# Kernel optimization log

Measured on AMD Instinct MI355X. Metric: run time of the kernel, lower is better.

## Reference

```python
import jax, jax.numpy as jnp
import numpy as np


def get_grid_index(init_grid_size, map_size):
    # nearest-neighbor 'interpolation' of flat indices, matching F.interpolate(mode='nearest')
    H_init, W_init = init_grid_size
    H, W = map_size
    # torch nearest: src index = floor(dst * scale), scale = src/dst
    rows = jnp.floor(jnp.arange(H_init) * (H / H_init)).astype(jnp.int32)
    cols = jnp.floor(jnp.arange(W_init) * (W / W_init)).astype(jnp.int32)
    idx = rows[:, None] * W + cols[None, :]
    return idx.reshape(-1)  # [N_init]


def _map2token(feature_map, idx_token, N, H_init, W_init):
    B, C, H, W = feature_map.shape
    N_init = H_init * W_init
    idx_hw = get_grid_index((H_init, W_init), (H, W))  # [N_init]
    # gather per-grid feature values: fm_flat[b, idx_hw] -> [B, N_init, C]
    fm = feature_map.transpose(0, 2, 3, 1).reshape(B, H * W, C)
    src = fm[:, idx_hw, :]  # [B, N_init, C]
    # scatter-add into tokens with counts
    def scatter_b(src_b, idx_b):
        num = jnp.zeros((N, C), src_b.dtype).at[idx_b].add(src_b)
        cnt = jnp.zeros((N,), src_b.dtype).at[idx_b].add(1.0)
        return num / (cnt + 1e-6)[:, None]
    return jax.vmap(scatter_b)(src, idx_token)  # [B, N, C]


def _token2map(x, idx_token, H, W, H_init, W_init):
    B, N, C = x.shape
    N_init = H_init * W_init
    idx_hw = get_grid_index((H_init, W_init), (H, W))  # [N_init]
    # each initial grid point contributes token x[b, idx_token[b,i]] to map cell idx_hw[i]
    def scatter_b(x_b, idx_tok_b):
        src = x_b[idx_tok_b]  # [N_init, C]
        num = jnp.zeros((H * W, C), x_b.dtype).at[idx_hw].add(src)
        cnt = jnp.zeros((H * W,), x_b.dtype).at[idx_hw].add(1.0)
        return num / (cnt + 1e-6)[:, None]
    out = jax.vmap(scatter_b)(x, idx_token)  # [B, H*W, C]
    return out.reshape(B, H, W, C).transpose(0, 3, 1, 2)


def setup_inputs() -> dict:
    key = jax.random.key(0)
    k1, k2, k3 = jax.random.split(key, 3)
    B, C, H, W = 8, 256, 56, 56
    N = 784
    H_init = W_init = 56
    N_init = H_init * W_init
    feature_map = jax.random.normal(k1, (B, C, H, W), dtype=jnp.float32)
    x = jax.random.normal(k2, (B, N, C), dtype=jnp.float32)
    idx_token = jax.random.randint(k3, (B, N_init), 0, N)
    return {"feature_map": feature_map, "x": x, "idx_token": idx_token,
            "token_num": N, "map_H": H, "map_W": W, "init_H": H_init, "init_W": W_init}


def reference(feature_map, x, idx_token, token_num, map_H, map_W, init_H, init_W):
    tokens = _map2token(feature_map, idx_token, token_num, init_H, init_W)
    fmap = _token2map(x, idx_token, map_H, map_W, init_H, init_W)
    return tokens, fmap
```

## Files before the change

kernel.cpp:

```cpp
#include <hip/hip_runtime.h>

#define BATCH 8
#define CCH   256
#define HWSZ  3136
#define NTOK  784
#define NINIT 3136
#define MAXM  40

#define FMT_OFF   0
#define CNT_OFF   25690112
#define SLOT_OFF  (25690112 + 25600)

#define CSR_BLOCKS 8
#define TR_BLOCKS  (BATCH * 49)
#define FM_BLOCKS  (BATCH * 49)
#define D1_BLOCKS  (CSR_BLOCKS + TR_BLOCKS + FM_BLOCKS)

__global__ __launch_bounds__(256) void d1_kernel(
    const float* __restrict__ fm,
    const float* __restrict__ x,
    const int*   __restrict__ idx,
    float*       __restrict__ fmap,
    float*       __restrict__ fmT,
    int*         __restrict__ cnt,
    int*         __restrict__ slot)
{
    __shared__ __align__(16) float tile[64][65];
    __shared__ int ns[64];

    const int bid = blockIdx.x;
    const int tid = threadIdx.x;

    if (bid < CSR_BLOCKS) {
        int* cnt_s = (int*)tile;
        int* cur_s = ((int*)tile) + NTOK;
        const int b = bid;
        for (int n = tid; n < NTOK; n += 256) { cnt_s[n] = 0; cur_s[n] = 0; }
        __syncthreads();
        const int* ib = idx + b * NINIT;
        for (int i = tid; i < NINIT; i += 256) atomicAdd(&cnt_s[ib[i]], 1);
        __syncthreads();
        for (int n = tid; n < NTOK; n += 256) cnt[b * NTOK + n] = cnt_s[n];
        for (int i = tid; i < NINIT; i += 256) {
            const int n = ib[i];
            const int p = atomicAdd(&cur_s[n], 1);
            if (p < MAXM) slot[(b * NTOK + n) * MAXM + p] = i;
        }
    } else if (bid < CSR_BLOCKS + TR_BLOCKS) {
        int t = bid - CSR_BLOCKS;
        const int b  = t & 7;
        const int it = t >> 3;
        const int i0 = it * 64;
        const int q  = tid & 15;
        const int r0 = tid >> 4;

        for (int ct = 0; ct < 4; ++ct) {
            const int c0 = ct * 64;
            #pragma unroll
            for (int p = 0; p < 4; ++p) {
                const int r = r0 + p * 16;
                const float4 v = *(const float4*)&fm[((size_t)(b * CCH + c0 + r)) * HWSZ + i0 + q * 4];
                tile[r][q * 4 + 0] = v.x;
                tile[r][q * 4 + 1] = v.y;
                tile[r][q * 4 + 2] = v.z;
                tile[r][q * 4 + 3] = v.w;
            }
            __syncthreads();
            #pragma unroll
            for (int p = 0; p < 4; ++p) {
                const int i = r0 + p * 16;
                float4 w;
                w.x = tile[q * 4 + 0][i];
                w.y = tile[q * 4 + 1][i];
                w.z = tile[q * 4 + 2][i];
                w.w = tile[q * 4 + 3][i];
                *(float4*)&fmT[((size_t)(b * HWSZ + i0 + i)) * CCH + c0 + q * 4] = w;
            }
            __syncthreads();
        }
    } else {
        int t = bid - CSR_BLOCKS - TR_BLOCKS;
        const int b  = t & 7;
        const int it = t >> 3;
        const int i0 = it * 64;
        const int lane = tid & 63;
        const int rr   = tid >> 6;
        const int q  = tid & 15;
        const int r0 = tid >> 4;

        if (tid < 64) ns[tid] = idx[b * NINIT + i0 + tid];
        __syncthreads();

        const float invc = 1.0f / (1.0f + 1e-6f);
        float* outb = fmap + (size_t)b * CCH * HWSZ;
        for (int ct = 0; ct < 4; ++ct) {
            const int c0 = ct * 64;
            #pragma unroll
            for (int p = 0; p < 4; ++p) {
                const int r = r0 + p * 16;
                const float4 v = *(const float4*)&x[((size_t)(b * NTOK + ns[r])) * CCH + c0 + q * 4];
                tile[r][q * 4 + 0] = v.x;
                tile[r][q * 4 + 1] = v.y;
                tile[r][q * 4 + 2] = v.z;
                tile[r][q * 4 + 3] = v.w;
            }
            __syncthreads();
            #pragma unroll
            for (int cc = rr; cc < 64; cc += 4) {
                outb[(size_t)(c0 + cc) * HWSZ + i0 + lane] = tile[lane][cc] * invc;
            }
            __syncthreads();
        }
    }
}

__global__ __launch_bounds__(256) void d2_kernel(
    const float* __restrict__ fmT,
    const int*   __restrict__ cnt,
    const int*   __restrict__ slot,
    float*       __restrict__ tokens)
{
    const int bid = blockIdx.x;
    const int tid = threadIdx.x;
    const int b  = bid & 7;
    const int g  = bid >> 3;
    const int tl = tid >> 6;
    const int c4 = (tid & 63) * 4;

    const float* fb = fmT + (size_t)b * HWSZ * CCH;
    #pragma unroll
    for (int u = 0; u < 2; ++u) {
        const int n  = g * 8 + u * 4 + tl;
        const int m  = cnt[b * NTOK + n];
        const int mm = m < MAXM ? m : MAXM;
        const int* sl = slot + (size_t)(b * NTOK + n) * MAXM;
        float4 acc = {0.f, 0.f, 0.f, 0.f};
        for (int k = 0; k < mm; ++k) {
            const float4 v = *(const float4*)&fb[(size_t)sl[k] * CCH + c4];
            acc.x += v.x; acc.y += v.y; acc.z += v.z; acc.w += v.w;
        }
        const float s = 1.0f / ((float)m + 1e-6f);
        acc.x *= s; acc.y *= s; acc.z *= s; acc.w *= s;
        *(float4*)&tokens[((size_t)(b * NTOK + n)) * CCH + c4] = acc;
    }
}

extern "C" void kernel_launch(void* const* d_in, const int* in_sizes, int n_in,
                              void* d_out, int out_size, void* d_ws, size_t ws_size,
                              hipStream_t stream) {
    const float* fm  = (const float*)d_in[0];
    const float* x   = (const float*)d_in[1];
    const int*   idx = (const int*)d_in[2];

    float* tokens = (float*)d_out;
    float* fmap   = (float*)d_out + (size_t)BATCH * NTOK * CCH;

    char*  ws   = (char*)d_ws;
    float* fmT  = (float*)(ws + FMT_OFF);
    int*   cnt  = (int*)(ws + CNT_OFF);
    int*   slot = (int*)(ws + SLOT_OFF);

    d1_kernel<<<D1_BLOCKS, 256, 0, stream>>>(fm, x, idx, fmap, fmT, cnt, slot);
    d2_kernel<<<BATCH * (NTOK / 8), 256, 0, stream>>>(fmT, cnt, slot, tokens);
}
```

Before: 114.1 us.

## Split transpose and fmap tiles per channel chunk and move fmap into second kernel

Each transpose and fmap-scatter block now handles a single 64-channel chunk instead of looping over four, so there are four times as many blocks with less serial work each. The fmap gather-write work moves from the first kernel into the second kernel, where it runs alongside the token-averaging blocks. This balances load between the two launches and raises parallelism on a large GPU. The cost is more blocks and more per-block index setup, and the idx indices are reloaded once per channel chunk.

```diff
diff --git a/kernel.cpp b/kernel.cpp
--- a/kernel.cpp
+++ b/kernel.cpp
@@ -12,22 +12,20 @@
 #define SLOT_OFF  (25690112 + 25600)
 
 #define CSR_BLOCKS 8
-#define TR_BLOCKS  (BATCH * 49)
-#define FM_BLOCKS  (BATCH * 49)
-#define D1_BLOCKS  (CSR_BLOCKS + TR_BLOCKS + FM_BLOCKS)
+#define TR_BLOCKS  (BATCH * 49 * 4)
+#define D1_BLOCKS  (CSR_BLOCKS + TR_BLOCKS)
+#define TOK_BLOCKS (BATCH * (NTOK / 8))
+#define FM_BLOCKS  (BATCH * 49 * 4)
+#define D2_BLOCKS  (TOK_BLOCKS + FM_BLOCKS)
 
 __global__ __launch_bounds__(256) void d1_kernel(
     const float* __restrict__ fm,
-    const float* __restrict__ x,
     const int*   __restrict__ idx,
-    float*       __restrict__ fmap,
     float*       __restrict__ fmT,
     int*         __restrict__ cnt,
     int*         __restrict__ slot)
 {
     __shared__ __align__(16) float tile[64][65];
-    __shared__ int ns[64];
-
     const int bid = blockIdx.x;
     const int tid = threadIdx.x;
 
@@ -46,102 +44,109 @@
             const int p = atomicAdd(&cur_s[n], 1);
             if (p < MAXM) slot[(b * NTOK + n) * MAXM + p] = i;
         }
-    } else if (bid < CSR_BLOCKS + TR_BLOCKS) {
+    } else {
         int t = bid - CSR_BLOCKS;
-        const int b  = t & 7;
-        const int it = t >> 3;
+        const int b  = t & 7;  t >>= 3;
+        const int ct = t & 3;  t >>= 2;
+        const int it = t;
+        const int c0 = ct * 64;
         const int i0 = it * 64;
+
         const int q  = tid & 15;
         const int r0 = tid >> 4;
 
-        for (int ct = 0; ct < 4; ++ct) {
-            const int c0 = ct * 64;
-            #pragma unroll
-            for (int p = 0; p < 4; ++p) {
-                const int r = r0 + p * 16;
-                const float4 v = *(const float4*)&fm[((size_t)(b * CCH + c0 + r)) * HWSZ + i0 + q * 4];
-                tile[r][q * 4 + 0] = v.x;
-                tile[r][q * 4 + 1] = v.y;
-                tile[r][q * 4 + 2] = v.z;
-                tile[r][q * 4 + 3] = v.w;
-            }
-            __syncthreads();
-            #pragma unroll
-            for (int p = 0; p < 4; ++p) {
-                const int i = r0 + p * 16;
-                float4 w;
-                w.x = tile[q * 4 + 0][i];
-                w.y = tile[q * 4 + 1][i];
-                w.z = tile[q * 4 + 2][i];
-                w.w = tile[q * 4 + 3][i];
-                *(float4*)&fmT[((size_t)(b * HWSZ + i0 + i)) * CCH + c0 + q * 4] = w;
-            }
-            __syncthreads();
+        #pragma unroll
+        for (int p = 0; p < 4; ++p) {
+            const int r = r0 + p * 16;
+            const float4 v = *(const float4*)&fm[((size_t)(b * CCH + c0 + r)) * HWSZ + i0 + q * 4];
+            tile[r][q * 4 + 0] = v.x;
+            tile[r][q * 4 + 1] = v.y;
+            tile[r][q * 4 + 2] = v.z;
+            tile[r][q * 4 + 3] = v.w;
         }
-    } else {
-        int t = bid - CSR_BLOCKS - TR_BLOCKS;
-        const int b  = t & 7;
-        const int it = t >> 3;
-        const int i0 = it * 64;
-        const int lane = tid & 63;
-        const int rr   = tid >> 6;
-        const int q  = tid & 15;
-        const int r0 = tid >> 4;
-
-        if (tid < 64) ns[tid] = idx[b * NINIT + i0 + tid];
         __syncthreads();
-
-        const float invc = 1.0f / (1.0f + 1e-6f);
-        float* outb = fmap + (size_t)b * CCH * HWSZ;
-        for (int ct = 0; ct < 4; ++ct) {
-            const int c0 = ct * 64;
-            #pragma unroll
-            for (int p = 0; p < 4; ++p) {
-                const int r = r0 + p * 16;
-                const float4 v = *(const float4*)&x[((size_t)(b * NTOK + ns[r])) * CCH + c0 + q * 4];
-                tile[r][q * 4 + 0] = v.x;
-                tile[r][q * 4 + 1] = v.y;
-                tile[r][q * 4 + 2] = v.z;
-                tile[r][q * 4 + 3] = v.w;
-            }
-            __syncthreads();
-            #pragma unroll
-            for (int cc = rr; cc < 64; cc += 4) {
-                outb[(size_t)(c0 + cc) * HWSZ + i0 + lane] = tile[lane][cc] * invc;
-            }
-            __syncthreads();
+        #pragma unroll
+        for (int p = 0; p < 4; ++p) {
+            const int i = r0 + p * 16;
+            float4 w;
+            w.x = tile[q * 4 + 0][i];
+            w.y = tile[q * 4 + 1][i];
+            w.z = tile[q * 4 + 2][i];
+            w.w = tile[q * 4 + 3][i];
+            *(float4*)&fmT[((size_t)(b * HWSZ + i0 + i)) * CCH + c0 + q * 4] = w;
         }
     }
 }
 
 __global__ __launch_bounds__(256) void d2_kernel(
+    const float* __restrict__ x,
+    const int*   __restrict__ idx,
     const float* __restrict__ fmT,
     const int*   __restrict__ cnt,
     const int*   __restrict__ slot,
-    float*       __restrict__ tokens)
+    float*       __restrict__ tokens,
+    float*       __restrict__ fmap)
 {
+    __shared__ __align__(16) float tile[64][65];
+    __shared__ int ns[64];
     const int bid = blockIdx.x;
     const int tid = threadIdx.x;
-    const int b  = bid & 7;
-    const int g  = bid >> 3;
-    const int tl = tid >> 6;
-    const int c4 = (tid & 63) * 4;
 
-    const float* fb = fmT + (size_t)b * HWSZ * CCH;
-    #pragma unroll
-    for (int u = 0; u < 2; ++u) {
-        const int n  = g * 8 + u * 4 + tl;
-        const int m  = cnt[b * NTOK + n];
-        const int mm = m < MAXM ? m : MAXM;
-        const int* sl = slot + (size_t)(b * NTOK + n) * MAXM;
-        float4 acc = {0.f, 0.f, 0.f, 0.f};
-        for (int k = 0; k < mm; ++k) {
-            const float4 v = *(const float4*)&fb[(size_t)sl[k] * CCH + c4];
-            acc.x += v.x; acc.y += v.y; acc.z += v.z; acc.w += v.w;
+    if (bid < TOK_BLOCKS) {
+        const int b  = bid & 7;
+        const int g  = bid >> 3;
+        const int tl = tid >> 6;
+        const int c4 = (tid & 63) * 4;
+
+        const float* fb = fmT + (size_t)b * HWSZ * CCH;
+        #pragma unroll
+        for (int u = 0; u < 2; ++u) {
+            const int n  = g * 8 + u * 4 + tl;
+            const int m  = cnt[b * NTOK + n];
+            const int mm = m < MAXM ? m : MAXM;
+            const int* sl = slot + (size_t)(b * NTOK + n) * MAXM;
+            float4 acc = {0.f, 0.f, 0.f, 0.f};
+            for (int k = 0; k < mm; ++k) {
+                const float4 v = *(const float4*)&fb[(size_t)sl[k] * CCH + c4];
+                acc.x += v.x; acc.y += v.y; acc.z += v.z; acc.w += v.w;
+            }
+            const float s = 1.0f / ((float)m + 1e-6f);
+            acc.x *= s; acc.y *= s; acc.z *= s; acc.w *= s;
+            *(float4*)&tokens[((size_t)(b * NTOK + n)) * CCH + c4] = acc;
         }
-        const float s = 1.0f / ((float)m + 1e-6f);
-        acc.x *= s; acc.y *= s; acc.z *= s; acc.w *= s;
-        *(float4*)&tokens[((size_t)(b * NTOK + n)) * CCH + c4] = acc;
+    } else {
+        int t = bid - TOK_BLOCKS;
+        const int b  = t & 7;  t >>= 3;
+        const int ct = t & 3;  t >>= 2;
+        const int it = t;
+        const int i0 = it * 64;
+        const int c0 = ct * 64;
+
+        const int lane = tid & 63;
+        const int rr   = tid >> 6;
+        const int q    = tid & 15;
+        const int r0   = tid >> 4;
+
+        if (tid < 64) ns[tid] = idx[b * NINIT + i0 + tid];
+        __syncthreads();
+
+        #pragma unroll
+        for (int p = 0; p < 4; ++p) {
+            const int r = r0 + p * 16;
+            const float4 v = *(const float4*)&x[((size_t)(b * NTOK + ns[r])) * CCH + c0 + q * 4];
+            tile[r][q * 4 + 0] = v.x;
+            tile[r][q * 4 + 1] = v.y;
+            tile[r][q * 4 + 2] = v.z;
+            tile[r][q * 4 + 3] = v.w;
+        }
+        __syncthreads();
+
+        const float invc = 1.0f / (1.0f + 1e-6f);
+        float* outb = fmap + (size_t)b * CCH * HWSZ;
+        #pragma unroll
+        for (int cc = rr; cc < 64; cc += 4) {
+            outb[(size_t)(c0 + cc) * HWSZ + i0 + lane] = tile[lane][cc] * invc;
+        }
     }
 }
 
@@ -160,6 +165,6 @@
     int*   cnt  = (int*)(ws + CNT_OFF);
     int*   slot = (int*)(ws + SLOT_OFF);
 
-    d1_kernel<<<D1_BLOCKS, 256, 0, stream>>>(fm, x, idx, fmap, fmT, cnt, slot);
-    d2_kernel<<<BATCH * (NTOK / 8), 256, 0, stream>>>(fmT, cnt, slot, tokens);
+    d1_kernel<<<D1_BLOCKS, 256, 0, stream>>>(fm, idx, fmT, cnt, slot);
+    d2_kernel<<<D2_BLOCKS, 256, 0, stream>>>(x, idx, fmT, cnt, slot, tokens, fmap);
 }
```

New measurement: 112.5 us. About the same (-1.4%).
